# Kernel tuning notes

Hardware: AMD Instinct MI355X
Metric: run time of the kernel (lower is better)

The kernel has to match this reference:

```python
import jax, jax.numpy as jnp
import numpy as np

N_NODES = 50000
N_EDGES = 800000
HEADS = 4
OUT_CH = 32
EDGE_EMB = 4
NEG_SLOPE = 0.2


def setup_inputs() -> dict:
    key = jax.random.key(0)
    ks = jax.random.split(key, 6)
    x = jax.random.normal(ks[0], (N_NODES, 128), dtype=jnp.float32)
    edge_index = jax.random.randint(ks[1], (2, N_EDGES), 0, N_NODES, dtype=jnp.int32)
    edge_attr = jax.random.normal(ks[2], (N_EDGES, 8), dtype=jnp.float32)
    W = jax.random.normal(ks[3], (128, HEADS * OUT_CH), dtype=jnp.float32) * 0.08
    We = jax.random.normal(ks[4], (8, HEADS * EDGE_EMB), dtype=jnp.float32) * 0.3
    att = jax.random.normal(ks[5], (1, HEADS, 2 * OUT_CH + EDGE_EMB), dtype=jnp.float32) * 0.1
    bias = jnp.zeros((HEADS * OUT_CH,), dtype=jnp.float32)
    return {"x": x, "edge_index": edge_index, "edge_attr": edge_attr,
            "W": W, "We": We, "att": att, "bias": bias}


def reference(x, edge_index, edge_attr, W, We, att, bias):
    # x: [N, Din], edge_index: [2, E] (row 0 = source j, row 1 = target i)
    src = edge_index[0]
    dst = edge_index[1]
    n = x.shape[0]

    xh = (x @ W).reshape(n, HEADS, OUT_CH)                    # [N, H, O]
    eh = (edge_attr @ We).reshape(-1, HEADS, EDGE_EMB)        # [E, H, P]

    a_i = att[0, :, :OUT_CH]                                  # [H, O]
    a_j = att[0, :, OUT_CH:2 * OUT_CH]                        # [H, O]
    a_e = att[0, :, 2 * OUT_CH:]                              # [H, P]

    # per-node dot with att halves, then gather per edge (avoids [E,H,O] concat)
    s_i = jnp.einsum('nho,ho->nh', xh, a_i)                   # [N, H]
    s_j = jnp.einsum('nho,ho->nh', xh, a_j)                   # [N, H]
    s_e = jnp.einsum('ehp,hp->eh', eh, a_e)                   # [E, H]

    alpha = s_i[dst] + s_j[src] + s_e                         # [E, H]
    alpha = jax.nn.leaky_relu(alpha, NEG_SLOPE)

    # segment softmax over incoming edges of each target node
    m = jax.ops.segment_max(alpha, dst, num_segments=n)       # [N, H]
    m = jnp.where(jnp.isfinite(m), m, 0.0)
    ea = jnp.exp(alpha - m[dst])                              # [E, H]
    denom = jax.ops.segment_sum(ea, dst, num_segments=n)      # [N, H]
    alpha = ea / (denom[dst] + 1e-16)                         # [E, H]

    msg = xh[src] * alpha[:, :, None]                         # [E, H, O]
    aggr = jax.ops.segment_sum(msg, dst, num_segments=n)      # [N, H, O]
    out = aggr.reshape(n, HEADS * OUT_CH) + bias              # concat heads
    return out
```

## Files before the change

kernel.cpp:

```cpp
#include <hip/hip_runtime.h>
#include <hip/hip_fp16.h>
#include <stdint.h>
#include <math.h>

#define NEG_SLOPE 0.2f

static __device__ __forceinline__ unsigned short f2bf(float f) {
    unsigned u = __float_as_uint(f);
    unsigned r = (u + 0x7FFFu + ((u >> 16) & 1u)) >> 16;
    return (unsigned short)r;
}
static __device__ __forceinline__ unsigned pack_h2(float a, float b) {
    __half2 h = __floats2half2_rn(a, b);
    return *(unsigned*)&h;
}

__global__ __launch_bounds__(256, 4) void k_gemm_scatter(
    const float* __restrict__ x, const float* __restrict__ W,
    const float* __restrict__ att, unsigned short* __restrict__ xh16,
    float* __restrict__ s_i, float* __restrict__ s_j, int n, int GB,
    const int* __restrict__ ei, const float* __restrict__ edge_attr,
    const float* __restrict__ We, int* __restrict__ cnt, int4* __restrict__ bucket,
    int slots, int E) {
    if (blockIdx.x >= GB) {
        __shared__ float ceS[32];
        int t = threadIdx.x;
        if (t < 32) {
            int k = t >> 2, h = t & 3;
            float s = 0.f;
            #pragma unroll
            for (int p = 0; p < 4; ++p)
                s += We[k * 16 + h * 4 + p] * att[h * 68 + 64 + p];
            ceS[t] = s;
        }
        __syncthreads();
        int e = (blockIdx.x - GB) * 256 + t;
        if (e < E) {
            float4 ea0 = *(const float4*)(edge_attr + (size_t)e * 8);
            float4 ea1 = *(const float4*)(edge_attr + (size_t)e * 8 + 4);
            float eav[8] = {ea0.x, ea0.y, ea0.z, ea0.w, ea1.x, ea1.y, ea1.z, ea1.w};
            float se[4];
            #pragma unroll
            for (int h = 0; h < 4; ++h) {
                float s = 0.f;
                #pragma unroll
                for (int k = 0; k < 8; ++k) s += eav[k] * ceS[k * 4 + h];
                se[h] = s;
            }
            int src = ei[e], dst = ei[E + e];
            int4 ent;
            ent.x = src;
            ent.y = (int)pack_h2(se[0], se[1]);
            ent.z = (int)pack_h2(se[2], se[3]);
            ent.w = 0;
            int p = atomicAdd(&cnt[dst], 1);
            if (p < slots) bucket[(size_t)dst * slots + p] = ent;
        }
        return;
    }
    __shared__ float wS[32 * 128];
    __shared__ float xS[64 * 32];
    int t = threadIdx.x;
    int c4 = t & 31;
    int rg = t >> 5;
    int r0 = blockIdx.x * 64;

    float acc[8][4];
    #pragma unroll
    for (int r = 0; r < 8; ++r)
        #pragma unroll
        for (int j = 0; j < 4; ++j) acc[r][j] = 0.f;

    for (int ch = 0; ch < 4; ++ch) {
        {
            const float4* Wv = (const float4*)(W + (size_t)ch * 32 * 128);
            #pragma unroll
            for (int i = 0; i < 4; ++i)
                ((float4*)wS)[t + i * 256] = Wv[t + i * 256];
        }
        #pragma unroll
        for (int i = 0; i < 2; ++i) {
            int idx = t + i * 256;
            int r = idx >> 3;
            int q = idx & 7;
            int row = r0 + r;
            float4 v = make_float4(0.f, 0.f, 0.f, 0.f);
            if (row < n) v = *(const float4*)(x + (size_t)row * 128 + ch * 32 + q * 4);
            ((float4*)xS)[idx] = v;
        }
        __syncthreads();
        #pragma unroll 1
        for (int q = 0; q < 8; ++q) {
            float wv[4][4];
            #pragma unroll
            for (int kk = 0; kk < 4; ++kk)
                #pragma unroll
                for (int j = 0; j < 4; ++j)
                    wv[kk][j] = wS[(4 * q + kk) * 128 + 32 * j + c4];
            #pragma unroll
            for (int r = 0; r < 8; ++r) {
                float4 xv = ((const float4*)xS)[(rg * 8 + r) * 8 + q];
                #pragma unroll
                for (int j = 0; j < 4; ++j)
                    acc[r][j] += xv.x * wv[0][j] + xv.y * wv[1][j]
                               + xv.z * wv[2][j] + xv.w * wv[3][j];
            }
        }
        __syncthreads();
    }

    float ai[4], aj[4];
    #pragma unroll
    for (int j = 0; j < 4; ++j) {
        ai[j] = att[j * 68 + c4];
        aj[j] = att[j * 68 + 32 + c4];
    }
    #pragma unroll 1
    for (int r = 0; r < 8; ++r) {
        int row = r0 + rg * 8 + r;
        bool ok = row < n;
        if (ok) {
            #pragma unroll
            for (int j = 0; j < 4; ++j)
                xh16[(size_t)row * 128 + c4 + 32 * j] = f2bf(acc[r][j]);
        }
        float p[8];
        #pragma unroll
        for (int j = 0; j < 4; ++j) {
            p[j] = acc[r][j] * ai[j];
            p[4 + j] = acc[r][j] * aj[j];
        }
        #pragma unroll
        for (int m = 1; m < 32; m <<= 1) {
            #pragma unroll
            for (int i = 0; i < 8; ++i) p[i] += __shfl_xor(p[i], m);
        }
        if (c4 == 0 && ok) {
            *(float4*)(s_i + (size_t)row * 4) = make_float4(p[0], p[1], p[2], p[3]);
            *(float4*)(s_j + (size_t)row * 4) = make_float4(p[4], p[5], p[6], p[7]);
        }
    }
}

__global__ __launch_bounds__(256) void k_aggr(
    const int* __restrict__ cnt, const int4* __restrict__ bucket, int slots,
    const float* __restrict__ s_i, const float* __restrict__ s_j,
    const unsigned* __restrict__ xh32, const float* __restrict__ bias,
    float* __restrict__ out, int n) {
    __shared__ float wbuf[4][64][4];
    __shared__ int sbuf[4][64];
    int wid = threadIdx.x >> 6;
    int l = threadIdx.x & 63;
    int node = blockIdx.x * 4 + wid;
    if (node >= n) return;
    int deg = cnt[node];
    deg = deg < slots ? deg : slots;
    float2 b = ((const float2*)bias)[l];
    float2* op = (float2*)(out + (size_t)node * 128);
    if (deg == 0) { op[l] = b; return; }

    float4 si4 = *(const float4*)(s_i + (size_t)node * 4);
    float lg[4];
    int src = 0;
    bool valid = l < deg;
    if (valid) {
        int4 ent = bucket[(size_t)node * slots + l];
        src = ent.x;
        float4 sj4 = *(const float4*)(s_j + (size_t)src * 4);
        __half2 se01 = *(__half2*)&ent.y;
        __half2 se23 = *(__half2*)&ent.z;
        float2 se01f = __half22float2(se01);
        float2 se23f = __half22float2(se23);
        float a;
        a = si4.x + sj4.x + se01f.x; lg[0] = a > 0.f ? a : NEG_SLOPE * a;
        a = si4.y + sj4.y + se01f.y; lg[1] = a > 0.f ? a : NEG_SLOPE * a;
        a = si4.z + sj4.z + se23f.x; lg[2] = a > 0.f ? a : NEG_SLOPE * a;
        a = si4.w + sj4.w + se23f.y; lg[3] = a > 0.f ? a : NEG_SLOPE * a;
    } else {
        lg[0] = lg[1] = lg[2] = lg[3] = -INFINITY;
    }
    float mx[4];
    #pragma unroll
    for (int h = 0; h < 4; ++h) mx[h] = lg[h];
    #pragma unroll
    for (int m = 1; m < 64; m <<= 1)
        #pragma unroll
        for (int h = 0; h < 4; ++h) mx[h] = fmaxf(mx[h], __shfl_xor(mx[h], m));
    float w[4], sm[4];
    #pragma unroll
    for (int h = 0; h < 4; ++h) {
        w[h] = valid ? __expf(lg[h] - mx[h]) : 0.f;
        sm[h] = w[h];
    }
    #pragma unroll
    for (int m = 1; m < 64; m <<= 1)
        #pragma unroll
        for (int h = 0; h < 4; ++h) sm[h] += __shfl_xor(sm[h], m);
    #pragma unroll
    for (int h = 0; h < 4; ++h) w[h] *= 1.f / (sm[h] + 1e-16f);

    *(float4*)&wbuf[wid][l][0] = make_float4(w[0], w[1], w[2], w[3]);
    sbuf[wid][l] = src;

    int hsel = l >> 4;
    float a0 = 0.f, a1 = 0.f;
    for (int j0 = 0; j0 < deg; j0 += 8) {
        int srcs[8];
        float ws[8];
        #pragma unroll
        for (int j = 0; j < 8; ++j) {
            int jj = j0 + j < deg ? j0 + j : 0;
            bool in = j0 + j < deg;
            srcs[j] = sbuf[wid][jj];
            ws[j] = in ? wbuf[wid][jj][hsel] : 0.f;
        }
        unsigned u[8];
        #pragma unroll
        for (int j = 0; j < 8; ++j) u[j] = xh32[(size_t)srcs[j] * 64 + l];
        #pragma unroll
        for (int j = 0; j < 8; ++j) {
            a0 += ws[j] * __uint_as_float(u[j] << 16);
            a1 += ws[j] * __uint_as_float(u[j] & 0xffff0000u);
        }
    }
    op[l] = make_float2(a0 + b.x, a1 + b.y);
}

extern "C" void kernel_launch(void* const* d_in, const int* in_sizes, int n_in,
                              void* d_out, int out_size, void* d_ws, size_t ws_size,
                              hipStream_t stream) {
    const float* x    = (const float*)d_in[0];
    const int*   ei   = (const int*)d_in[1];
    const float* eattr= (const float*)d_in[2];
    const float* W    = (const float*)d_in[3];
    const float* We   = (const float*)d_in[4];
    const float* att  = (const float*)d_in[5];
    const float* bias = (const float*)d_in[6];
    float* out = (float*)d_out;
    int n = in_sizes[0] / 128;
    int E = in_sizes[1] / 2;

    char* w = (char*)d_ws;
    auto alloc = [&](size_t bytes) {
        char* p = w;
        w += (bytes + 255) & ~(size_t)255;
        return (void*)p;
    };
    unsigned short* xh16 = (unsigned short*)alloc((size_t)n * 128 * 2);
    float* s_i           = (float*)alloc((size_t)n * 16);
    float* s_j           = (float*)alloc((size_t)n * 16);
    int* cnt             = (int*)alloc((size_t)n * 4);
    size_t remain = (ws_size > (size_t)(w - (char*)d_ws))
                  ? ws_size - (size_t)(w - (char*)d_ws) : 0;
    int slots = (int)(remain / ((size_t)n * 16));
    if (slots > 64) slots = 64;
    if (slots < 32) slots = 32;
    int4* bucket         = (int4*)alloc((size_t)n * slots * 16);

    int GB = (n + 63) / 64;
    int EB = (E + 255) / 256;

    (void)hipMemsetAsync(cnt, 0, (size_t)n * 4, stream);
    k_gemm_scatter<<<GB + EB, 256, 0, stream>>>(x, W, att, xh16, s_i, s_j, n, GB,
                                                ei, eattr, We, cnt, bucket, slots, E);
    k_aggr<<<(n + 3) / 4, 256, 0, stream>>>(cnt, bucket, slots, s_i, s_j,
                                            (const unsigned*)xh16, bias, out, n);
}
```

Measured before the change: 191.9 us.

## Precompute W·att projection, batch edge loads, widen gather unroll, fuse memset

Adds an init kernel that folds the attention vectors into W (a 128x8 Wa matrix) and zeroes the counters, replacing the memset. The GEMM accumulates the s_i/s_j scores directly through an extra accumulator, removing the per-row shuffle reductions. Edge-scatter blocks now each handle four edges per thread with loads issued up front, and the aggregation loop gathers 16 neighbours per iteration instead of 8. The extra kernel launch and higher register pressure are the costs.

After: 210.4 us. +9.6%, slower.

```diff
diff --git a/kernel.cpp b/kernel.cpp
--- a/kernel.cpp
+++ b/kernel.cpp
@@ -15,9 +15,31 @@
     return *(unsigned*)&h;
 }
 
+__global__ __launch_bounds__(256) void k_init(const float* __restrict__ W,
+                                              const float* __restrict__ att,
+                                              float* __restrict__ Wa,
+                                              int* __restrict__ cnt, int n) {
+    int t = threadIdx.x;
+    if (blockIdx.x == 0) {
+        for (int i = t; i < 1024; i += 256) {
+            int k = i >> 3, c = i & 7, h = c & 3;
+            const float* a = att + h * 68 + ((c & 4) ? 32 : 0);
+            const float* wp = W + k * 128 + h * 32;
+            float s = 0.f;
+            #pragma unroll
+            for (int o = 0; o < 32; ++o) s += wp[o] * a[o];
+            Wa[i] = s;
+        }
+    } else {
+        int i = (blockIdx.x - 1) * 256 + t;
+        if (i < n) cnt[i] = 0;
+    }
+}
+
 __global__ __launch_bounds__(256, 4) void k_gemm_scatter(
     const float* __restrict__ x, const float* __restrict__ W,
-    const float* __restrict__ att, unsigned short* __restrict__ xh16,
+    const float* __restrict__ Wa, const float* __restrict__ att,
+    unsigned short* __restrict__ xh16,
     float* __restrict__ s_i, float* __restrict__ s_j, int n, int GB,
     const int* __restrict__ ei, const float* __restrict__ edge_attr,
     const float* __restrict__ We, int* __restrict__ cnt, int4* __restrict__ bucket,
@@ -34,11 +56,25 @@
             ceS[t] = s;
         }
         __syncthreads();
-        int e = (blockIdx.x - GB) * 256 + t;
-        if (e < E) {
-            float4 ea0 = *(const float4*)(edge_attr + (size_t)e * 8);
-            float4 ea1 = *(const float4*)(edge_attr + (size_t)e * 8 + 4);
-            float eav[8] = {ea0.x, ea0.y, ea0.z, ea0.w, ea1.x, ea1.y, ea1.z, ea1.w};
+        int base = (blockIdx.x - GB) * 1024 + t;
+        int srcs[4], dsts[4];
+        float4 ea0[4], ea1[4];
+        #pragma unroll
+        for (int it = 0; it < 4; ++it) {
+            int e = base + it * 256;
+            if (e < E) {
+                srcs[it] = ei[e];
+                dsts[it] = ei[E + e];
+                ea0[it] = *(const float4*)(edge_attr + (size_t)e * 8);
+                ea1[it] = *(const float4*)(edge_attr + (size_t)e * 8 + 4);
+            }
+        }
+        #pragma unroll
+        for (int it = 0; it < 4; ++it) {
+            int e = base + it * 256;
+            if (e >= E) continue;
+            float eav[8] = {ea0[it].x, ea0[it].y, ea0[it].z, ea0[it].w,
+                            ea1[it].x, ea1[it].y, ea1[it].z, ea1[it].w};
             float se[4];
             #pragma unroll
             for (int h = 0; h < 4; ++h) {
@@ -47,29 +83,32 @@
                 for (int k = 0; k < 8; ++k) s += eav[k] * ceS[k * 4 + h];
                 se[h] = s;
             }
-            int src = ei[e], dst = ei[E + e];
             int4 ent;
-            ent.x = src;
+            ent.x = srcs[it];
             ent.y = (int)pack_h2(se[0], se[1]);
             ent.z = (int)pack_h2(se[2], se[3]);
             ent.w = 0;
-            int p = atomicAdd(&cnt[dst], 1);
-            if (p < slots) bucket[(size_t)dst * slots + p] = ent;
+            int p = atomicAdd(&cnt[dsts[it]], 1);
+            if (p < slots) bucket[(size_t)dsts[it] * slots + p] = ent;
         }
         return;
     }
     __shared__ float wS[32 * 128];
     __shared__ float xS[64 * 32];
+    __shared__ float wA[32 * 8];
     int t = threadIdx.x;
     int c4 = t & 31;
     int rg = t >> 5;
     int r0 = blockIdx.x * 64;
 
     float acc[8][4];
-    #pragma unroll
-    for (int r = 0; r < 8; ++r)
+    float acc2[8];
+    #pragma unroll
+    for (int r = 0; r < 8; ++r) {
+        acc2[r] = 0.f;
         #pragma unroll
         for (int j = 0; j < 4; ++j) acc[r][j] = 0.f;
+    }
 
     for (int ch = 0; ch < 4; ++ch) {
         {
@@ -78,6 +117,7 @@
             for (int i = 0; i < 4; ++i)
                 ((float4*)wS)[t + i * 256] = Wv[t + i * 256];
         }
+        wA[t] = Wa[ch * 256 + t];
         #pragma unroll
         for (int i = 0; i < 2; ++i) {
             int idx = t + i * 256;
@@ -97,6 +137,13 @@
                 #pragma unroll
                 for (int j = 0; j < 4; ++j)
                     wv[kk][j] = wS[(4 * q + kk) * 128 + 32 * j + c4];
+            float wa0 = 0.f, wa1 = 0.f, wa2 = 0.f, wa3 = 0.f;
+            if (c4 < 8) {
+                wa0 = wA[(4 * q + 0) * 8 + c4];
+                wa1 = wA[(4 * q + 1) * 8 + c4];
+                wa2 = wA[(4 * q + 2) * 8 + c4];
+                wa3 = wA[(4 * q + 3) * 8 + c4];
+            }
             #pragma unroll
             for (int r = 0; r < 8; ++r) {
                 float4 xv = ((const float4*)xS)[(rg * 8 + r) * 8 + q];
@@ -104,40 +151,23 @@
                 for (int j = 0; j < 4; ++j)
                     acc[r][j] += xv.x * wv[0][j] + xv.y * wv[1][j]
                                + xv.z * wv[2][j] + xv.w * wv[3][j];
+                acc2[r] += xv.x * wa0 + xv.y * wa1 + xv.z * wa2 + xv.w * wa3;
             }
         }
         __syncthreads();
     }
 
-    float ai[4], aj[4];
-    #pragma unroll
-    for (int j = 0; j < 4; ++j) {
-        ai[j] = att[j * 68 + c4];
-        aj[j] = att[j * 68 + 32 + c4];
-    }
     #pragma unroll 1
     for (int r = 0; r < 8; ++r) {
         int row = r0 + rg * 8 + r;
-        bool ok = row < n;
-        if (ok) {
+        if (row < n) {
             #pragma unroll
             for (int j = 0; j < 4; ++j)
                 xh16[(size_t)row * 128 + c4 + 32 * j] = f2bf(acc[r][j]);
-        }
-        float p[8];
-        #pragma unroll
-        for (int j = 0; j < 4; ++j) {
-            p[j] = acc[r][j] * ai[j];
-            p[4 + j] = acc[r][j] * aj[j];
-        }
-        #pragma unroll
-        for (int m = 1; m < 32; m <<= 1) {
-            #pragma unroll
-            for (int i = 0; i < 8; ++i) p[i] += __shfl_xor(p[i], m);
-        }
-        if (c4 == 0 && ok) {
-            *(float4*)(s_i + (size_t)row * 4) = make_float4(p[0], p[1], p[2], p[3]);
-            *(float4*)(s_j + (size_t)row * 4) = make_float4(p[4], p[5], p[6], p[7]);
+            if (c4 < 8) {
+                float* sp = (c4 < 4) ? s_i : s_j;
+                sp[(size_t)row * 4 + (c4 & 3)] = acc2[r];
+            }
         }
     }
 }
@@ -204,21 +234,21 @@
 
     int hsel = l >> 4;
     float a0 = 0.f, a1 = 0.f;
-    for (int j0 = 0; j0 < deg; j0 += 8) {
-        int srcs[8];
-        float ws[8];
-        #pragma unroll
-        for (int j = 0; j < 8; ++j) {
-            int jj = j0 + j < deg ? j0 + j : 0;
+    for (int j0 = 0; j0 < deg; j0 += 16) {
+        int srcs[16];
+        float ws[16];
+        #pragma unroll
+        for (int j = 0; j < 16; ++j) {
             bool in = j0 + j < deg;
+            int jj = in ? j0 + j : 0;
             srcs[j] = sbuf[wid][jj];
             ws[j] = in ? wbuf[wid][jj][hsel] : 0.f;
         }
-        unsigned u[8];
-        #pragma unroll
-        for (int j = 0; j < 8; ++j) u[j] = xh32[(size_t)srcs[j] * 64 + l];
-        #pragma unroll
-        for (int j = 0; j < 8; ++j) {
+        unsigned u[16];
+        #pragma unroll
+        for (int j = 0; j < 16; ++j) u[j] = xh32[(size_t)srcs[j] * 64 + l];
+        #pragma unroll
+        for (int j = 0; j < 16; ++j) {
             a0 += ws[j] * __uint_as_float(u[j] << 16);
             a1 += ws[j] * __uint_as_float(u[j] & 0xffff0000u);
         }
@@ -250,6 +280,7 @@
     float* s_i           = (float*)alloc((size_t)n * 16);
     float* s_j           = (float*)alloc((size_t)n * 16);
     int* cnt             = (int*)alloc((size_t)n * 4);
+    float* Wa            = (float*)alloc(128 * 8 * 4);
     size_t remain = (ws_size > (size_t)(w - (char*)d_ws))
                   ? ws_size - (size_t)(w - (char*)d_ws) : 0;
     int slots = (int)(remain / ((size_t)n * 16));
@@ -258,10 +289,10 @@
     int4* bucket         = (int4*)alloc((size_t)n * slots * 16);
 
     int GB = (n + 63) / 64;
-    int EB = (E + 255) / 256;
-
-    (void)hipMemsetAsync(cnt, 0, (size_t)n * 4, stream);
-    k_gemm_scatter<<<GB + EB, 256, 0, stream>>>(x, W, att, xh16, s_i, s_j, n, GB,
+    int EB = (E + 1023) / 1024;
+
+    k_init<<<1 + (n + 255) / 256, 256, 0, stream>>>(W, att, Wa, cnt, n);
+    k_gemm_scatter<<<GB + EB, 256, 0, stream>>>(x, W, Wa, att, xh16, s_i, s_j, n, GB,
                                                 ei, eattr, We, cnt, bucket, slots, E);
     k_aggr<<<(n + 3) / 4, 256, 0, stream>>>(cnt, bucket, slots, s_i, s_j,
                                             (const unsigned*)xh16, bias, out, n);
```
